# Kernel tuning notes

Hardware: AMD Instinct MI355X
Metric: run time of the kernel (lower is better)

## Reference

```python
import jax, jax.numpy as jnp
import numpy as np

# dims: batch, q-heads, kv-heads, seq, head_dim, block size, window (kv blocks per q block)
B, H, KVH, S, D = 2, 16, 4, 4096, 64
BLK, W = 64, 8
G = H // KVH          # heads per group = 4
NQ = S // BLK         # 64 query blocks
L = W * BLK           # flattened kv window per q block = 512


def setup_inputs() -> dict:
    key = jax.random.key(0)
    k0, k1, k2, k3 = jax.random.split(key, 4)
    q = jax.random.normal(k0, (B, H, S, D), jnp.float32)
    k = jax.random.normal(k1, (B, KVH, S, D), jnp.float32)
    v = jax.random.normal(k2, (B, KVH, S, D), jnp.float32)
    # standard alibi slopes 2^(-8i/H)
    alibi_slopes = jnp.asarray(2.0 ** (-8.0 * np.arange(1, H + 1) / H), jnp.float32)
    # contiguous segments via sorted random ids
    segment_ids = jnp.sort(jax.random.randint(k3, (B, S), 0, 8, jnp.int32), axis=-1)
    # causal sliding window: q block qb attends to kv blocks [qb-W+1, qb]; -1 = invalid
    qb = np.arange(NQ)[:, None]
    bi = qb - (W - 1) + np.arange(W)[None, :]
    block_indices = jnp.asarray(np.where(bi < 0, -1, bi), jnp.int32)  # [NQ, W]
    return {"q": q, "k": k, "v": v, "alibi_slopes": alibi_slopes,
            "segment_ids": segment_ids, "block_indices": block_indices}


def reference(q, k, v, alibi_slopes, segment_ids, block_indices):
    scale = jnp.float32(1.0 / np.sqrt(D))
    NEG = jnp.float32(-1e30)

    qg = q.reshape(B, KVH, G, NQ, BLK, D)          # GQA grouping
    kb = k.reshape(B, KVH, NQ, BLK, D)
    vb = v.reshape(B, KVH, NQ, BLK, D)

    safe = jnp.clip(block_indices, 0)               # [NQ, W]
    kg = kb[:, :, safe]                             # [B,KVH,NQ,W,BLK,D] gathered kv blocks
    vg = vb[:, :, safe]

    pos_m = (jnp.arange(NQ) * BLK)[:, None] + jnp.arange(BLK)             # [NQ,BM]
    pos_n = safe[:, :, None] * BLK + jnp.arange(BLK)[None, None, :]       # [NQ,W,BN]

    valid = (block_indices >= 0)[:, None, :, None]                        # [NQ,1,W,1]
    causal = pos_m[:, :, None, None] >= pos_n[:, None, :, :]              # [NQ,BM,W,BN]
    seg_q = segment_ids.reshape(B, NQ, BLK)
    seg_k = jnp.take(segment_ids, pos_n.reshape(-1), axis=1).reshape(B, NQ, W, BLK)
    same_seg = (seg_q[:, :, :, None, None] == seg_k[:, :, None, :, :]) & (seg_q[:, :, :, None, None] >= 0)
    mask = ((valid & causal)[None] & same_seg)                            # [B,NQ,BM,W,BN]
    maskb = mask.reshape(B, 1, 1, NQ, BLK, L)                             # broadcast over KVH,G

    scores = jnp.einsum('bkgqmd,bkqwnd->bkgqmwn', qg, kg) * scale         # [B,KVH,G,NQ,BM,W,BN]
    pos_diff = jnp.abs(pos_m[:, :, None, None] - pos_n[:, None, :, :]).astype(jnp.float32)
    scores = scores - alibi_slopes.reshape(KVH, G)[None, :, :, None, None, None, None] * pos_diff
    scores = scores.reshape(B, KVH, G, NQ, BLK, L)
    scores = jnp.where(maskb, scores, NEG)

    row_max = jnp.max(scores, axis=-1, keepdims=True)
    p = jnp.where(maskb, jnp.exp(scores - row_max), 0.0)
    l = jnp.sum(p, axis=-1, keepdims=True)                                # [B,KVH,G,NQ,BM,1]
    vf = vg.reshape(B, KVH, NQ, L, D)
    acc = jnp.einsum('bkgqml,bkqld->bkgqmd', p, vf)
    out = jnp.where(l > 0, acc / jnp.where(l > 0, l, 1.0), 0.0)           # zero rows with no valid kv
    return out.reshape(B, H, S, D)
```

## Files before the change

kernel.cpp:

```cpp
#include <hip/hip_runtime.h>
#include <hip/hip_bf16.h>

#define NKVH 4
#define SEQ 4096
#define BLK 64
#define NW 8
#define NQB 64

typedef __attribute__((ext_vector_type(8))) short bf16x8;
typedef __attribute__((ext_vector_type(4))) float f32x4;

__device__ __forceinline__ unsigned pkbf(unsigned lo, unsigned hi) {
  return __builtin_amdgcn_perm(hi + 0x8000u, lo + 0x8000u, 0x07060302u);
}

__device__ __forceinline__ void gload16(const void* g, void* l) {
  __builtin_amdgcn_global_load_lds(
      (const __attribute__((address_space(1))) void*)g,
      (__attribute__((address_space(3))) void*)l, 16, 0, 0);
}

__global__ __launch_bounds__(256, 2)
void prep_kernel(const float* __restrict__ kp, const float* __restrict__ vp,
                 const int* __restrict__ seg,
                 short* __restrict__ kw, short* __restrict__ vt,
                 int* __restrict__ fo)
{
  const int ki = blockIdx.x, kvh = blockIdx.y, b = blockIdx.z;
  const size_t base = (((size_t)(b*NKVH + kvh)*SEQ) + (size_t)ki*BLK)*64;
  __shared__ float sk[64][72];
  __shared__ float sv[64][72];
  __shared__ int fol[8];
  const int t = threadIdx.x;
  #pragma unroll
  for (int it = 0; it < 4; ++it) {
    const int i = t + it*256;
    const int row = i >> 4, c4 = i & 15;
    float4 a = *(const float4*)(kp + base + row*64 + c4*4);
    *(float4*)&sk[row][c4*4] = a;
    float4 v = *(const float4*)(vp + base + row*64 + c4*4);
    *(float4*)&sv[row][c4*4] = v;
  }
  if (ki == 0 && kvh == 0 && t < 8) fol[t] = 0x7FFFFFFF;
  __syncthreads();
  #pragma unroll
  for (int it = 0; it < 2; ++it) {
    const int o = t + it*256;
    const int s = o >> 8, fd = (o >> 6) & 3, lg = (o >> 4) & 3, lr = o & 15;
    const int krow = 8*(lr >> 2) + (lr & 3) + 4*(fd & 1) + 32*(fd >> 1);
    const float* src = &sk[krow][s*32 + lg*8];
    uint4 w;
    w.x = pkbf(__float_as_uint(src[0]), __float_as_uint(src[1]));
    w.y = pkbf(__float_as_uint(src[2]), __float_as_uint(src[3]));
    w.z = pkbf(__float_as_uint(src[4]), __float_as_uint(src[5]));
    w.w = pkbf(__float_as_uint(src[6]), __float_as_uint(src[7]));
    *(uint4*)(kw + base + (size_t)o*8) = w;
    const int d = fd*16 + lr;
    const int n0 = s*32 + lg*8;
    uint4 u;
    u.x = pkbf(__float_as_uint(sv[n0+0][d]), __float_as_uint(sv[n0+1][d]));
    u.y = pkbf(__float_as_uint(sv[n0+2][d]), __float_as_uint(sv[n0+3][d]));
    u.z = pkbf(__float_as_uint(sv[n0+4][d]), __float_as_uint(sv[n0+5][d]));
    u.w = pkbf(__float_as_uint(sv[n0+6][d]), __float_as_uint(sv[n0+7][d]));
    *(uint4*)(vt + base + (size_t)o*8) = u;
  }
  if (ki == 0 && kvh == 0) {
    for (int i = t; i < SEQ; i += 256) {
      const int v = seg[b*SEQ + i];
      if (i == 0 || seg[b*SEQ + i - 1] != v) atomicMin(&fol[v], i);
    }
    __syncthreads();
    if (t < 8) fo[b*8 + t] = fol[t];
  }
}

__global__ __launch_bounds__(256, 2)
void sattn_kernel(const float* __restrict__ qp, const short* __restrict__ kw,
                  const short* __restrict__ vt, const float* __restrict__ alibi,
                  const int* __restrict__ seg, const int* __restrict__ bidx,
                  const int* __restrict__ fo, float* __restrict__ outp)
{
  const int raw = blockIdx.x;
  const int xcd = raw & 7, li = raw >> 3;
  const int b = xcd >> 2, kvh = xcd & 3;
  const int qb = li & 63, hp = li >> 6;

  const int tid = threadIdx.x;
  const int wave = tid >> 6, lane = tid & 63;
  const int lr = lane & 15, lg = lane >> 4;
  const int wh = wave & 1, wq = wave >> 1;
  const int head = kvh*4 + hp*2 + wh;

  __shared__ short klds[2][4096];
  __shared__ short vlds[2][4096];

  int kis[NW];
  #pragma unroll
  for (int i = 0; i < NW; ++i) kis[i] = bidx[qb*NW + i];

  int m_glob[2], lo[2];
  unsigned relm[2];
  #pragma unroll
  for (int g = 0; g < 2; ++g) {
    m_glob[g] = qb*BLK + (wq*2 + g)*16 + lr;
    const int sv = seg[b*SEQ + m_glob[g]];
    lo[g] = fo[b*8 + sv];
    relm[g] = (unsigned)(m_glob[g] - lo[g]);
  }
  const float LOG2E = 1.4426950408889634f;
  const float nslope = -alibi[head] * LOG2E;
  float nsr[4];
  #pragma unroll
  for (int r = 0; r < 4; ++r) nsr[r] = -nslope * (float)r;

  const short* kbase = kw + ((size_t)(b*NKVH + kvh)*SEQ)*64;
  const short* vbase = vt + ((size_t)(b*NKVH + kvh)*SEQ)*64;

  auto STAGE = [&](int buf, int wi) {
    const int ki = kis[wi] < 0 ? 0 : kis[wi];
    const char* ksrc = (const char*)(kbase + (size_t)ki*4096);
    const char* vsrc = (const char*)(vbase + (size_t)ki*4096);
    gload16(ksrc + tid*16,        (char*)&klds[buf][0] + wave*1024);
    gload16(ksrc + 4096 + tid*16, (char*)&klds[buf][0] + 4096 + wave*1024);
    gload16(vsrc + tid*16,        (char*)&vlds[buf][0] + wave*1024);
    gload16(vsrc + 4096 + tid*16, (char*)&vlds[buf][0] + 4096 + wave*1024);
  };

  STAGE(0, 0);

  bf16x8 qf[2][2];
  {
    const float qs = 0.125f * LOG2E;
    #pragma unroll
    for (int g = 0; g < 2; ++g) {
      const float* qrow = qp + (((size_t)b*16 + head)*SEQ + m_glob[g])*64;
      #pragma unroll
      for (int s = 0; s < 2; ++s) {
        float4 a = *(const float4*)(qrow + s*32 + lg*8);
        float4 c = *(const float4*)(qrow + s*32 + lg*8 + 4);
        union { unsigned u[4]; bf16x8 v; } cv;
        cv.u[0] = pkbf(__float_as_uint(a.x*qs), __float_as_uint(a.y*qs));
        cv.u[1] = pkbf(__float_as_uint(a.z*qs), __float_as_uint(a.w*qs));
        cv.u[2] = pkbf(__float_as_uint(c.x*qs), __float_as_uint(c.y*qs));
        cv.u[3] = pkbf(__float_as_uint(c.z*qs), __float_as_uint(c.w*qs));
        qf[g][s] = cv.v;
      }
    }
  }

  union { unsigned short us[8]; bf16x8 v; } one_u;
  #pragma unroll
  for (int i = 0; i < 8; ++i) one_u.us[i] = 0x3F80;
  const bf16x8 onesf = one_u.v;

  f32x4 oacc[2][4], osum[2];
  #pragma unroll
  for (int g = 0; g < 2; ++g) {
    f32x4 z = {0.f,0.f,0.f,0.f};
    osum[g] = z;
    #pragma unroll
    for (int dt = 0; dt < 4; ++dt) oacc[g][dt] = z;
  }

  asm volatile("s_waitcnt vmcnt(0)" ::: "memory");
  __builtin_amdgcn_s_barrier();

  #pragma unroll
  for (int wi = 0; wi < NW; ++wi) {
    const int cur = wi & 1;
    if (wi + 1 < NW) STAGE(cur ^ 1, wi + 1);
    const int kvi = kis[wi];
    if (kvi >= 0) {
      f32x4 sacc[2][4];
      #pragma unroll
      for (int g = 0; g < 2; ++g)
        #pragma unroll
        for (int f = 0; f < 4; ++f) { f32x4 z = {0.f,0.f,0.f,0.f}; sacc[g][f] = z; }
      #pragma unroll
      for (int s = 0; s < 2; ++s) {
        bf16x8 kf[4];
        #pragma unroll
        for (int f = 0; f < 4; ++f)
          kf[f] = *(const bf16x8*)&klds[cur][(s*256 + f*64 + lane)*8];
        __builtin_amdgcn_s_setprio(1);
        #pragma unroll
        for (int f = 0; f < 4; ++f)
          sacc[0][f] = __builtin_amdgcn_mfma_f32_16x16x32_bf16(kf[f], qf[0][s], sacc[0][f], 0, 0, 0);
        #pragma unroll
        for (int f = 0; f < 4; ++f)
          sacc[1][f] = __builtin_amdgcn_mfma_f32_16x16x32_bf16(kf[f], qf[1][s], sacc[1][f], 0, 0, 0);
        __builtin_amdgcn_s_setprio(0);
      }

      unsigned pk[2][4][2];
      #pragma unroll
      for (int g = 0; g < 2; ++g) {
        #pragma unroll
        for (int f = 0; f < 4; ++f) {
          const int nb = lg*8 + 4*(f & 1) + 32*(f >> 1);
          const int n0 = kvi*BLK + nb;
          const unsigned nrel0 = (unsigned)(n0 - lo[g]);
          const float af = nslope * (float)(m_glob[g] - n0);
          float p[4];
          #pragma unroll
          for (int r = 0; r < 4; ++r) {
            const bool live = (nrel0 + (unsigned)r) <= relm[g];
            const float pv = __builtin_amdgcn_exp2f(sacc[g][f][r] + af + nsr[r]);
            p[r] = live ? pv : 0.f;
          }
          pk[g][f][0] = pkbf(__float_as_uint(p[0]), __float_as_uint(p[1]));
          pk[g][f][1] = pkbf(__float_as_uint(p[2]), __float_as_uint(p[3]));
        }
      }

      #pragma unroll
      for (int s = 0; s < 2; ++s) {
        bf16x8 vf[4];
        #pragma unroll
        for (int dt = 0; dt < 4; ++dt)
          vf[dt] = *(const bf16x8*)&vlds[cur][(s*256 + dt*64 + lane)*8];
        union { unsigned u[4]; bf16x8 v; } pf0, pf1;
        pf0.u[0] = pk[0][2*s][0]; pf0.u[1] = pk[0][2*s][1];
        pf0.u[2] = pk[0][2*s+1][0]; pf0.u[3] = pk[0][2*s+1][1];
        pf1.u[0] = pk[1][2*s][0]; pf1.u[1] = pk[1][2*s][1];
        pf1.u[2] = pk[1][2*s+1][0]; pf1.u[3] = pk[1][2*s+1][1];
        __builtin_amdgcn_s_setprio(1);
        #pragma unroll
        for (int dt = 0; dt < 4; ++dt)
          oacc[0][dt] = __builtin_amdgcn_mfma_f32_16x16x32_bf16(vf[dt], pf0.v, oacc[0][dt], 0, 0, 0);
        #pragma unroll
        for (int dt = 0; dt < 4; ++dt)
          oacc[1][dt] = __builtin_amdgcn_mfma_f32_16x16x32_bf16(vf[dt], pf1.v, oacc[1][dt], 0, 0, 0);
        osum[0] = __builtin_amdgcn_mfma_f32_16x16x32_bf16(onesf, pf0.v, osum[0], 0, 0, 0);
        osum[1] = __builtin_amdgcn_mfma_f32_16x16x32_bf16(onesf, pf1.v, osum[1], 0, 0, 0);
        __builtin_amdgcn_s_setprio(0);
      }
    }
    if (wi + 1 < NW) {
      asm volatile("s_waitcnt vmcnt(0)" ::: "memory");
      __builtin_amdgcn_s_barrier();
    }
  }

  #pragma unroll
  for (int g = 0; g < 2; ++g) {
    const float lrow = osum[g][0];
    const float inv = lrow > 0.f ? 1.f/lrow : 0.f;
    float* dst = outp + (((size_t)b*16 + head)*SEQ + m_glob[g])*64;
    #pragma unroll
    for (int dt = 0; dt < 4; ++dt) {
      float4 o;
      o.x = oacc[g][dt][0]*inv; o.y = oacc[g][dt][1]*inv;
      o.z = oacc[g][dt][2]*inv; o.w = oacc[g][dt][3]*inv;
      *(float4*)&dst[dt*16 + lg*4] = o;
    }
  }
}

extern "C" void kernel_launch(void* const* d_in, const int* in_sizes, int n_in,
                              void* d_out, int out_size, void* d_ws, size_t ws_size,
                              hipStream_t stream) {
  const float* q    = (const float*)d_in[0];
  const float* k    = (const float*)d_in[1];
  const float* v    = (const float*)d_in[2];
  const float* al   = (const float*)d_in[3];
  const int*   sg   = (const int*)d_in[4];
  const int*   bi   = (const int*)d_in[5];
  short* kws  = (short*)d_ws;
  short* vtws = (short*)((char*)d_ws + (size_t)(1u<<22));
  int*   fo   = (int*)((char*)d_ws + (size_t)(1u<<23));
  dim3 pgrid(NQB, NKVH, 2);
  prep_kernel<<<pgrid, 256, 0, stream>>>(k, v, sg, kws, vtws, fo);
  sattn_kernel<<<dim3(1024), 256, 0, stream>>>(q, kws, vtws, al, sg, bi, fo, (float*)d_out);
}
```

Measured before the change: 49.31 us.

## Share KV staging across all four group heads and parallelize segment-start scan

The attention kernel now launches 512 workgroups of 512 threads, each covering all four query heads of a KV group for one query block, instead of two heads per workgroup. Each K/V window block is therefore staged into LDS once per group rather than twice. The segment-start computation moves out of one serial workgroup and is spread across all prep workgroups with global atomicMin, initialised by a memset. The trade-off is fewer, larger workgroups, which may lower occupancy and latency hiding, plus one extra memset launch.

```diff
diff --git a/kernel.cpp b/kernel.cpp
--- a/kernel.cpp
+++ b/kernel.cpp
@@ -30,7 +30,6 @@
   const size_t base = (((size_t)(b*NKVH + kvh)*SEQ) + (size_t)ki*BLK)*64;
   __shared__ float sk[64][72];
   __shared__ float sv[64][72];
-  __shared__ int fol[8];
   const int t = threadIdx.x;
   #pragma unroll
   for (int it = 0; it < 4; ++it) {
@@ -41,7 +40,12 @@
     float4 v = *(const float4*)(vp + base + row*64 + c4*4);
     *(float4*)&sv[row][c4*4] = v;
   }
-  if (ki == 0 && kvh == 0 && t < 8) fol[t] = 0x7FFFFFFF;
+  if (kvh == 0 && t < BLK) {
+    const int idx = ki*BLK + t;
+    const int v = seg[b*SEQ + idx];
+    const bool bnd = (idx == 0) || (seg[b*SEQ + idx - 1] != v);
+    if (bnd) atomicMin(&fo[b*8 + v], idx);
+  }
   __syncthreads();
   #pragma unroll
   for (int it = 0; it < 2; ++it) {
@@ -64,32 +68,23 @@
     u.w = pkbf(__float_as_uint(sv[n0+6][d]), __float_as_uint(sv[n0+7][d]));
     *(uint4*)(vt + base + (size_t)o*8) = u;
   }
-  if (ki == 0 && kvh == 0) {
-    for (int i = t; i < SEQ; i += 256) {
-      const int v = seg[b*SEQ + i];
-      if (i == 0 || seg[b*SEQ + i - 1] != v) atomicMin(&fol[v], i);
-    }
-    __syncthreads();
-    if (t < 8) fo[b*8 + t] = fol[t];
-  }
-}
-
-__global__ __launch_bounds__(256, 2)
+}
+
+__global__ __launch_bounds__(512, 2)
 void sattn_kernel(const float* __restrict__ qp, const short* __restrict__ kw,
                   const short* __restrict__ vt, const float* __restrict__ alibi,
                   const int* __restrict__ seg, const int* __restrict__ bidx,
                   const int* __restrict__ fo, float* __restrict__ outp)
 {
   const int raw = blockIdx.x;
-  const int xcd = raw & 7, li = raw >> 3;
+  const int xcd = raw & 7, qb = raw >> 3;
   const int b = xcd >> 2, kvh = xcd & 3;
-  const int qb = li & 63, hp = li >> 6;
 
   const int tid = threadIdx.x;
   const int wave = tid >> 6, lane = tid & 63;
   const int lr = lane & 15, lg = lane >> 4;
-  const int wh = wave & 1, wq = wave >> 1;
-  const int head = kvh*4 + hp*2 + wh;
+  const int wh = wave & 3, wq2 = wave >> 2;
+  const int head = kvh*4 + wh;
 
   __shared__ short klds[2][4096];
   __shared__ short vlds[2][4096];
@@ -102,7 +97,7 @@
   unsigned relm[2];
   #pragma unroll
   for (int g = 0; g < 2; ++g) {
-    m_glob[g] = qb*BLK + (wq*2 + g)*16 + lr;
+    m_glob[g] = qb*BLK + (wq2*2 + g)*16 + lr;
     const int sv = seg[b*SEQ + m_glob[g]];
     lo[g] = fo[b*8 + sv];
     relm[g] = (unsigned)(m_glob[g] - lo[g]);
@@ -118,12 +113,10 @@
 
   auto STAGE = [&](int buf, int wi) {
     const int ki = kis[wi] < 0 ? 0 : kis[wi];
-    const char* ksrc = (const char*)(kbase + (size_t)ki*4096);
-    const char* vsrc = (const char*)(vbase + (size_t)ki*4096);
-    gload16(ksrc + tid*16,        (char*)&klds[buf][0] + wave*1024);
-    gload16(ksrc + 4096 + tid*16, (char*)&klds[buf][0] + 4096 + wave*1024);
-    gload16(vsrc + tid*16,        (char*)&vlds[buf][0] + wave*1024);
-    gload16(vsrc + 4096 + tid*16, (char*)&vlds[buf][0] + 4096 + wave*1024);
+    gload16((const char*)(kbase + (size_t)ki*4096) + tid*16,
+            (char*)&klds[buf][0] + tid*16);
+    gload16((const char*)(vbase + (size_t)ki*4096) + tid*16,
+            (char*)&vlds[buf][0] + tid*16);
   };
 
   STAGE(0, 0);
@@ -269,7 +262,8 @@
   short* kws  = (short*)d_ws;
   short* vtws = (short*)((char*)d_ws + (size_t)(1u<<22));
   int*   fo   = (int*)((char*)d_ws + (size_t)(1u<<23));
+  hipMemsetAsync(fo, 0x7F, 64, stream);
   dim3 pgrid(NQB, NKVH, 2);
   prep_kernel<<<pgrid, 256, 0, stream>>>(k, v, sg, kws, vtws, fo);
-  sattn_kernel<<<dim3(1024), 256, 0, stream>>>(q, kws, vtws, al, sg, bi, fo, (float*)d_out);
-}
+  sattn_kernel<<<dim3(512), 512, 0, stream>>>(q, kws, vtws, al, sg, bi, fo, (float*)d_out);
+}
```

Measured after the change: 51.95 us. 1.05x slower.
